# Performance work log

Measured on AMD Instinct MI355X. Metric: run time of the kernel, lower is better.

## Reference

```python
import jax, jax.numpy as jnp
import numpy as np

D = 1024        # d_hidden
DE = 512        # d_expert (routed)
E = 8           # n_routed_experts
TOP_K = 2
DS = DE * 2     # shared expert width = d_expert * n_shared_experts


def setup_inputs() -> dict:
    key = jax.random.key(0)
    ks = jax.random.split(key, 8)
    s = 1.0 / np.sqrt(D)
    return {
        "x": jax.random.normal(ks[0], (2, 1024, D), dtype=jnp.float32),
        "W_g": jax.random.normal(ks[1], (D, E), dtype=jnp.float32) * s,
        "Wg_e": jax.random.normal(ks[2], (E, D, DE), dtype=jnp.float32) * s,
        "Wu_e": jax.random.normal(ks[3], (E, D, DE), dtype=jnp.float32) * s,
        "Wd_e": jax.random.normal(ks[4], (E, DE, D), dtype=jnp.float32) * (1.0 / np.sqrt(DE)),
        "Wg_s": jax.random.normal(ks[5], (D, DS), dtype=jnp.float32) * s,
        "Wu_s": jax.random.normal(ks[6], (D, DS), dtype=jnp.float32) * s,
        "Wd_s": jax.random.normal(ks[7], (DS, D), dtype=jnp.float32) * (1.0 / np.sqrt(DS)),
    }


def _moe(x, W_g, Wg_e, Wu_e, Wd_e, Wg_s, Wu_s, Wd_s):
    B, T, Dm = x.shape
    N = B * T
    xf = x.reshape(N, Dm)

    # shared expert (SwiGLU)
    shared = (jax.nn.silu(xf @ Wg_s) * (xf @ Wu_s)) @ Wd_s  # [N, D]

    # gating: softmax then top-k (set membership identical to torch sorted=False)
    probs = jax.nn.softmax(xf @ W_g, axis=-1)               # [N, E]
    topk_vals, topk_ids = jax.lax.top_k(probs, TOP_K)       # [N, K]

    # combine weights c[n, e] = sum of topk_vals where routed to expert e
    # (equivalent to the original gather -> weighted scatter_add combine)
    c = jnp.zeros((N, E), dtype=x.dtype)
    c = c.at[jnp.arange(N)[:, None], topk_ids].add(topk_vals)

    # dense per-expert SwiGLU, weighted-combined (same math as gather/scatter loop)
    gate = jax.nn.silu(jnp.einsum('nd,edh->neh', xf, Wg_e))
    up = jnp.einsum('nd,edh->neh', xf, Wu_e)
    routed = jnp.einsum('neh,ne,ehd->nd', gate * up, c, Wd_e)  # [N, D]

    return (shared + routed).reshape(B, T, Dm)


def reference(x, W_g, Wg_e, Wu_e, Wd_e, Wg_s, Wu_s, Wd_s):
    return _moe(x, W_g, Wg_e, Wu_e, Wd_e, Wg_s, Wu_s, Wd_s)
```

## Files before the change

kernel.cpp:

```cpp
#include <hip/hip_runtime.h>
#include <hip/hip_bf16.h>

#define NTOK 2048
#define DIM  1024
#define DEXP 512
#define NEXP 8
#define DSH  1024
#define KH   5120
#define MAXROWS 5120

typedef __hip_bfloat16 bf16;
typedef __attribute__((ext_vector_type(8))) short bf16x8;
typedef __attribute__((ext_vector_type(4))) float floatx4;

__device__ __forceinline__ void gl_lds16(const bf16* g, bf16* l) {
    __builtin_amdgcn_global_load_lds(
        (const __attribute__((address_space(1))) void*)g,
        (__attribute__((address_space(3))) void*)l, 16, 0, 0);
}

__device__ __forceinline__ float b2f(short s) {
    union { float f; unsigned u; } v;
    v.u = ((unsigned)(unsigned short)s) << 16;
    return v.f;
}

struct B4 { bf16 a, b, c, d; };

__global__ __launch_bounds__(256) void gate_logits(const float* __restrict__ x,
                                                   const float* __restrict__ Wg,
                                                   bf16* __restrict__ Xb,
                                                   int2* __restrict__ te,
                                                   float2* __restrict__ tp) {
    int t = blockIdx.x * 4 + (threadIdx.x >> 6);
    int lane = threadIdx.x & 63;
    const float* xr = x + (long)t * DIM;
    bf16* xo = Xb + (long)t * DIM;
    float acc[NEXP] = {0.f, 0.f, 0.f, 0.f, 0.f, 0.f, 0.f, 0.f};
#pragma unroll
    for (int i = 0; i < 4; i++) {
        int d = lane * 4 + i * 256;
        float4 xv = *(const float4*)(xr + d);
        B4 o{__float2bfloat16(xv.x), __float2bfloat16(xv.y),
             __float2bfloat16(xv.z), __float2bfloat16(xv.w)};
        *(B4*)(xo + d) = o;
#pragma unroll
        for (int j = 0; j < 4; j++) {
            float xs = (j == 0) ? xv.x : (j == 1) ? xv.y : (j == 2) ? xv.z : xv.w;
            float4 w0 = *(const float4*)(Wg + (d + j) * NEXP);
            float4 w1 = *(const float4*)(Wg + (d + j) * NEXP + 4);
            acc[0] += xs * w0.x; acc[1] += xs * w0.y; acc[2] += xs * w0.z; acc[3] += xs * w0.w;
            acc[4] += xs * w1.x; acc[5] += xs * w1.y; acc[6] += xs * w1.z; acc[7] += xs * w1.w;
        }
    }
#pragma unroll
    for (int e = 0; e < NEXP; e++)
#pragma unroll
        for (int off = 32; off; off >>= 1)
            acc[e] += __shfl_xor(acc[e], off);
    if (lane == 0) {
        float m = acc[0];
#pragma unroll
        for (int e = 1; e < NEXP; e++) m = fmaxf(m, acc[e]);
        float p[NEXP], s = 0.f;
#pragma unroll
        for (int e = 0; e < NEXP; e++) { p[e] = expf(acc[e] - m); s += p[e]; }
        float inv = 1.f / s;
#pragma unroll
        for (int e = 0; e < NEXP; e++) p[e] *= inv;
        int i1 = 0;
#pragma unroll
        for (int e = 1; e < NEXP; e++) if (p[e] > p[i1]) i1 = e;
        int i2 = (i1 == 0) ? 1 : 0;
#pragma unroll
        for (int e = 0; e < NEXP; e++) if (e != i1 && p[e] > p[i2]) i2 = e;
        te[t] = make_int2(i1, i2);
        tp[t] = make_float2(p[i1], p[i2]);
    }
}

__global__ __launch_bounds__(512) void assign_kernel(const int2* __restrict__ te,
                                                     const float2* __restrict__ tp,
                                                     int* __restrict__ counts,
                                                     int* __restrict__ offs,
                                                     int* __restrict__ tok_list,
                                                     float* __restrict__ cw,
                                                     int* __restrict__ s1a,
                                                     int* __restrict__ s2a) {
    __shared__ int cnt[NEXP];
    const int e = threadIdx.x >> 6;
    const int lane = threadIdx.x & 63;
    int base = 0;
    for (int t0 = 0; t0 < NTOK; t0 += 64) {
        int t = t0 + lane;
        int2 ee = te[t];
        bool m1 = (ee.x == e), m2 = (ee.y == e);
        bool mt = m1 || m2;
        unsigned long long mask = __ballot(mt);
        int pre = __popcll(mask & ((1ull << lane) - 1ull));
        if (mt) {
            int slot = base + pre;
            tok_list[e * NTOK + slot] = t;
            float2 pp = tp[t];
            cw[e * NTOK + slot] = m1 ? pp.x : pp.y;
            if (m1) s1a[t] = slot; else s2a[t] = slot;
        }
        base += __popcll(mask);
    }
    if (lane == 0) cnt[e] = base;
    __syncthreads();
    if (threadIdx.x == 0) {
        int o = 0;
#pragma unroll
        for (int i = 0; i < NEXP; i++) {
            counts[i] = cnt[i];
            offs[i] = o;
            o += (cnt[i] + 127) & ~127;
        }
    }
}

__global__ __launch_bounds__(256) void pack_weights(
        const float* __restrict__ Wg_s, const float* __restrict__ Wu_s,
        const float* __restrict__ Wg_e, const float* __restrict__ Wu_e,
        const float* __restrict__ Wd_s, const float* __restrict__ Wd_e,
        bf16* __restrict__ Bg, bf16* __restrict__ Bu, bf16* __restrict__ Bd) {
    __shared__ float t[32][36];
    int b = blockIdx.x;
    const float* src; bf16* dst; int C; long dstStride, dstBase; int tilesX;
    if (b < 1024)       { src = Wg_s; dst = Bg; C = 1024; dstStride = 1024; dstBase = 0; tilesX = 32; }
    else if (b < 2048)  { b -= 1024; src = Wu_s; dst = Bu; C = 1024; dstStride = 1024; dstBase = 0; tilesX = 32; }
    else if (b < 6144)  { b -= 2048; int z = b >> 9; b &= 511;
                          src = Wg_e + (long)z * DIM * DEXP; dst = Bg; C = 512;
                          dstStride = 1024; dstBase = (long)(DSH + z * DEXP) * 1024; tilesX = 16; }
    else if (b < 10240) { b -= 6144; int z = b >> 9; b &= 511;
                          src = Wu_e + (long)z * DIM * DEXP; dst = Bu; C = 512;
                          dstStride = 1024; dstBase = (long)(DSH + z * DEXP) * 1024; tilesX = 16; }
    else if (b < 11264) { b -= 10240; src = Wd_s; dst = Bd; C = 1024; dstStride = KH; dstBase = 0; tilesX = 32; }
    else                { b -= 11264; int z = b >> 9; b &= 511;
                          src = Wd_e + (long)z * DEXP * DIM; dst = Bd; C = 1024;
                          dstStride = KH; dstBase = DSH + (long)z * DEXP; tilesX = 32; }
    int tileX = b & (tilesX - 1), tileY = b / tilesX;
    int c0 = tileX * 32, r0 = tileY * 32;

    {
        int row = threadIdx.x >> 3, ch = threadIdx.x & 7;
        float4 v = *(const float4*)(src + (long)(r0 + row) * C + c0 + ch * 4);
        *(float4*)(&t[row][ch * 4]) = v;
    }
    __syncthreads();
    {
        int dc = threadIdx.x & 31, ch = threadIdx.x >> 5;
        int j = ch * 4;
        B4 o{__float2bfloat16(t[j][dc]), __float2bfloat16(t[j + 1][dc]),
             __float2bfloat16(t[j + 2][dc]), __float2bfloat16(t[j + 3][dc])};
        *(B4*)(dst + dstBase + (long)(c0 + dc) * dstStride + r0 + j) = o;
    }
}

__global__ __launch_bounds__(256) void gu_all(const bf16* __restrict__ X,
                                              const bf16* __restrict__ Bg,
                                              const bf16* __restrict__ Bu,
                                              const int* __restrict__ counts,
                                              const int* __restrict__ offs,
                                              const int* __restrict__ tok_list,
                                              const float* __restrict__ cw,
                                              bf16* __restrict__ Hs,
                                              bf16* __restrict__ He) {
    __shared__ __align__(16) bf16 sA[128 * 32];
    __shared__ __align__(16) bf16 sBg[64 * 32];
    __shared__ __align__(16) bf16 sBu[64 * 32];

    const int b = blockIdx.x;
    const bool routed = b < 1024;
    int e = 0, m, c;
    if (routed) {
        e = b >> 7; m = (b >> 3) & 15; c = b & 7;
        if (m * 128 >= counts[e]) return;
    } else {
        int bs = b - 1024; m = bs >> 4; c = bs & 15;
    }
    const int so = routed ? offs[e] : 0;
    const int colB0 = routed ? (DSH + e * DEXP + c * 64) : c * 64;

    const int tid = threadIdx.x;
    const int wave = tid >> 6, lane = tid & 63;
    const int wr = wave >> 1, wc = wave & 1;
    const int q = lane >> 4, l15 = lane & 15;
    const int koff = (q ^ ((l15 >> 1) & 3)) * 8;

    const int r0 = tid >> 2, c4 = tid & 3;
    const int r1 = r0 + 64;
    const int c4s = c4 ^ ((r0 >> 1) & 3);
    long aRow0, aRow1;
    if (routed) {
        const int* tl = tok_list + e * NTOK + m * 128;
        aRow0 = (long)tl[r0] * DIM;
        aRow1 = (long)tl[r1] * DIM;
    } else {
        aRow0 = (long)(m * 128 + r0) * DIM;
        aRow1 = (long)(m * 128 + r1) * DIM;
    }
    const long bRow = (long)(colB0 + r0) * DIM;

    floatx4 accG[4][2], accU[4][2];
    const floatx4 z4 = {0.f, 0.f, 0.f, 0.f};
#pragma unroll
    for (int i = 0; i < 4; i++)
#pragma unroll
        for (int j = 0; j < 2; j++) { accG[i][j] = z4; accU[i][j] = z4; }

    for (int k0 = 0; k0 < DIM; k0 += 32) {
        gl_lds16(X + aRow0 + k0 + c4s * 8, sA + (wave * 64) * 8);
        gl_lds16(X + aRow1 + k0 + c4s * 8, sA + (256 + wave * 64) * 8);
        gl_lds16(Bg + bRow + k0 + c4s * 8, sBg + (wave * 64) * 8);
        gl_lds16(Bu + bRow + k0 + c4s * 8, sBu + (wave * 64) * 8);
        __syncthreads();

        bf16x8 af[4], bg[2], bu[2];
#pragma unroll
        for (int rt = 0; rt < 4; rt++)
            af[rt] = *(const bf16x8*)(sA + (wr * 64 + rt * 16 + l15) * 32 + koff);
#pragma unroll
        for (int ct = 0; ct < 2; ct++) {
            int cb = (wc * 32 + ct * 16 + l15) * 32 + koff;
            bg[ct] = *(const bf16x8*)(sBg + cb);
            bu[ct] = *(const bf16x8*)(sBu + cb);
        }
#pragma unroll
        for (int rt = 0; rt < 4; rt++)
#pragma unroll
            for (int ct = 0; ct < 2; ct++) {
                accG[rt][ct] = __builtin_amdgcn_mfma_f32_16x16x32_bf16(af[rt], bg[ct], accG[rt][ct], 0, 0, 0);
                accU[rt][ct] = __builtin_amdgcn_mfma_f32_16x16x32_bf16(af[rt], bu[ct], accU[rt][ct], 0, 0, 0);
            }
        __syncthreads();
    }

    float wv[4][4];
#pragma unroll
    for (int rt = 0; rt < 4; rt++)
#pragma unroll
        for (int r = 0; r < 4; r++) {
            int srow = wr * 64 + rt * 16 + q * 4 + r;
            wv[rt][r] = routed ? cw[e * NTOK + m * 128 + srow] : 1.0f;
        }
#pragma unroll
    for (int rt = 0; rt < 4; rt++)
#pragma unroll
        for (int ct = 0; ct < 2; ct++)
#pragma unroll
            for (int r = 0; r < 4; r++) {
                int srow = wr * 64 + rt * 16 + q * 4 + r;
                int colLoc = c * 64 + wc * 32 + ct * 16 + l15;
                float g = accG[rt][ct][r];
                float u = accU[rt][ct][r];
                float h = (g / (1.f + __expf(-g))) * u * wv[rt][r];
                if (routed)
                    He[(long)(so + m * 128 + srow) * DEXP + colLoc] = __float2bfloat16(h);
                else
                    Hs[(long)(m * 128 + srow) * DSH + colLoc] = __float2bfloat16(h);
            }
}

__global__ __launch_bounds__(256) void down_all(const bf16* __restrict__ Hs,
                                                const bf16* __restrict__ He,
                                                const bf16* __restrict__ Bd,
                                                const int* __restrict__ counts,
                                                const int* __restrict__ offs,
                                                bf16* __restrict__ Ys,
                                                bf16* __restrict__ Ye) {
    __shared__ __align__(16) bf16 sA[128 * 32];
    __shared__ __align__(16) bf16 sB[64 * 32];

    const int b = blockIdx.x;
    const bool routed = b < 2048;
    int e = 0, m, cc;
    if (routed) {
        e = b >> 8; m = (b >> 4) & 15; cc = b & 15;
        if (m * 128 >= counts[e]) return;
    } else {
        int bs = b - 2048; m = bs >> 4; cc = bs & 15;
    }
    const int so = routed ? offs[e] : 0;
    const bf16* A = routed ? He + (long)so * DEXP : Hs;
    bf16* Y = routed ? Ye + (long)so * DIM : Ys;
    const int astr = routed ? DEXP : DSH;
    const int ksteps = routed ? (DEXP / 32) : (DSH / 32);
    const int kg0 = routed ? (DSH + e * DEXP) : 0;

    const int tid = threadIdx.x;
    const int wave = tid >> 6, lane = tid & 63;
    const int wr = wave >> 1, wc = wave & 1;
    const int q = lane >> 4, l15 = lane & 15;
    const int koff = (q ^ ((l15 >> 1) & 3)) * 8;

    const int r0 = tid >> 2, c4 = tid & 3;
    const int r1 = r0 + 64;
    const int c4s = c4 ^ ((r0 >> 1) & 3);
    const long aRow0 = (long)(m * 128 + r0) * astr;
    const long aRow1 = (long)(m * 128 + r1) * astr;
    const long bRow = (long)(cc * 64 + r0) * KH + kg0;

    floatx4 acc[4][2];
    const floatx4 z4 = {0.f, 0.f, 0.f, 0.f};
#pragma unroll
    for (int i = 0; i < 4; i++)
#pragma unroll
        for (int j = 0; j < 2; j++) acc[i][j] = z4;

    for (int ks = 0; ks < ksteps; ks++) {
        const int k0 = ks * 32;
        gl_lds16(A + aRow0 + k0 + c4s * 8, sA + (wave * 64) * 8);
        gl_lds16(A + aRow1 + k0 + c4s * 8, sA + (256 + wave * 64) * 8);
        gl_lds16(Bd + bRow + k0 + c4s * 8, sB + (wave * 64) * 8);
        __syncthreads();

        bf16x8 af[4], bb[2];
#pragma unroll
        for (int rt = 0; rt < 4; rt++)
            af[rt] = *(const bf16x8*)(sA + (wr * 64 + rt * 16 + l15) * 32 + koff);
#pragma unroll
        for (int ct = 0; ct < 2; ct++)
            bb[ct] = *(const bf16x8*)(sB + (wc * 32 + ct * 16 + l15) * 32 + koff);
#pragma unroll
        for (int rt = 0; rt < 4; rt++)
#pragma unroll
            for (int ct = 0; ct < 2; ct++)
                acc[rt][ct] = __builtin_amdgcn_mfma_f32_16x16x32_bf16(af[rt], bb[ct], acc[rt][ct], 0, 0, 0);
        __syncthreads();
    }

#pragma unroll
    for (int rt = 0; rt < 4; rt++)
#pragma unroll
        for (int ct = 0; ct < 2; ct++)
#pragma unroll
            for (int r = 0; r < 4; r++) {
                int srow = wr * 64 + rt * 16 + q * 4 + r;
                int mc = cc * 64 + wc * 32 + ct * 16 + l15;
                Y[(long)(m * 128 + srow) * DIM + mc] = __float2bfloat16(acc[rt][ct][r]);
            }
}

__global__ __launch_bounds__(256) void combine_kernel(const bf16* __restrict__ Ys,
                                                      const bf16* __restrict__ Ye,
                                                      const int2* __restrict__ te,
                                                      const int* __restrict__ s1a,
                                                      const int* __restrict__ s2a,
                                                      const int* __restrict__ offs,
                                                      float* __restrict__ out) {
    int idx = blockIdx.x * 256 + threadIdx.x;
    int t = idx >> 7;
    int d = (idx & 127) * 8;
    int2 ee = te[t];
    long r1 = (long)(offs[ee.x] + s1a[t]);
    long r2 = (long)(offs[ee.y] + s2a[t]);
    bf16x8 a = *(const bf16x8*)(Ys + (long)t * DIM + d);
    bf16x8 p = *(const bf16x8*)(Ye + r1 * DIM + d);
    bf16x8 r = *(const bf16x8*)(Ye + r2 * DIM + d);
    float* o = out + (long)t * DIM + d;
#pragma unroll
    for (int i = 0; i < 8; i++)
        o[i] = b2f(a[i]) + b2f(p[i]) + b2f(r[i]);
}

extern "C" void kernel_launch(void* const* d_in, const int* in_sizes, int n_in,
                              void* d_out, int out_size, void* d_ws, size_t ws_size,
                              hipStream_t stream) {
    const float* x    = (const float*)d_in[0];
    const float* W_g  = (const float*)d_in[1];
    const float* Wg_e = (const float*)d_in[2];
    const float* Wu_e = (const float*)d_in[3];
    const float* Wd_e = (const float*)d_in[4];
    const float* Wg_s = (const float*)d_in[5];
    const float* Wu_s = (const float*)d_in[6];
    const float* Wd_s = (const float*)d_in[7];
    float* out = (float*)d_out;

    bf16* Xb = (bf16*)d_ws;
    bf16* Bg = Xb + (size_t)NTOK * DIM;
    bf16* Bu = Bg + (size_t)KH * DIM;
    bf16* Bd = Bu + (size_t)KH * DIM;
    bf16* Hs = Bd + (size_t)DIM * KH;
    bf16* He = Hs + (size_t)NTOK * DSH;
    bf16* Ys = He + (size_t)MAXROWS * DEXP;
    bf16* Ye = Ys + (size_t)NTOK * DIM;
    int*  counts   = (int*)(Ye + (size_t)MAXROWS * DIM);
    int*  offs     = counts + NEXP;
    int*  tok_list = offs + NEXP;
    float* cw      = (float*)(tok_list + NEXP * NTOK);
    int*  s1a      = (int*)(cw + NEXP * NTOK);
    int*  s2a      = s1a + NTOK;
    int2* te       = (int2*)(s2a + NTOK);
    float2* tp     = (float2*)(te + NTOK);

    hipMemsetAsync(tok_list, 0,
                   sizeof(int) * NEXP * NTOK + sizeof(float) * NEXP * NTOK, stream);
    gate_logits<<<NTOK / 4, 256, 0, stream>>>(x, W_g, Xb, te, tp);
    assign_kernel<<<1, 512, 0, stream>>>(te, tp, counts, offs, tok_list, cw, s1a, s2a);
    pack_weights<<<15360, 256, 0, stream>>>(Wg_s, Wu_s, Wg_e, Wu_e, Wd_s, Wd_e, Bg, Bu, Bd);
    gu_all<<<1280, 256, 0, stream>>>(Xb, Bg, Bu, counts, offs, tok_list, cw, Hs, He);
    down_all<<<2304, 256, 0, stream>>>(Hs, He, Bd, counts, offs, Ys, Ye);
    combine_kernel<<<NTOK * DIM / 8 / 256, 256, 0, stream>>>(Ys, Ye, te, s1a, s2a, offs, out);
}
```

Before: 208.5 us.

## Double GEMM K-tile to 64, merge gating with weight packing, drop memset

Fuses the gating/softmax/top-k kernel and the weight transpose-pack kernel into a single launch. The memset of the token list is dropped; assign_kernel now zeroes only the padding slots of each expert segment. Both grouped GEMMs move from a K-tile of 32 to 64 with a new 8-way XOR LDS swizzle. This halves the barrier count per K step and issues more async loads per sync, at the cost of twice the LDS per block.

```diff
diff --git a/kernel.cpp b/kernel.cpp
--- a/kernel.cpp
+++ b/kernel.cpp
@@ -27,55 +27,90 @@
 
 struct B4 { bf16 a, b, c, d; };
 
-__global__ __launch_bounds__(256) void gate_logits(const float* __restrict__ x,
-                                                   const float* __restrict__ Wg,
-                                                   bf16* __restrict__ Xb,
-                                                   int2* __restrict__ te,
-                                                   float2* __restrict__ tp) {
-    int t = blockIdx.x * 4 + (threadIdx.x >> 6);
-    int lane = threadIdx.x & 63;
-    const float* xr = x + (long)t * DIM;
-    bf16* xo = Xb + (long)t * DIM;
-    float acc[NEXP] = {0.f, 0.f, 0.f, 0.f, 0.f, 0.f, 0.f, 0.f};
-#pragma unroll
-    for (int i = 0; i < 4; i++) {
-        int d = lane * 4 + i * 256;
-        float4 xv = *(const float4*)(xr + d);
-        B4 o{__float2bfloat16(xv.x), __float2bfloat16(xv.y),
-             __float2bfloat16(xv.z), __float2bfloat16(xv.w)};
-        *(B4*)(xo + d) = o;
-#pragma unroll
-        for (int j = 0; j < 4; j++) {
-            float xs = (j == 0) ? xv.x : (j == 1) ? xv.y : (j == 2) ? xv.z : xv.w;
-            float4 w0 = *(const float4*)(Wg + (d + j) * NEXP);
-            float4 w1 = *(const float4*)(Wg + (d + j) * NEXP + 4);
-            acc[0] += xs * w0.x; acc[1] += xs * w0.y; acc[2] += xs * w0.z; acc[3] += xs * w0.w;
-            acc[4] += xs * w1.x; acc[5] += xs * w1.y; acc[6] += xs * w1.z; acc[7] += xs * w1.w;
-        }
-    }
-#pragma unroll
-    for (int e = 0; e < NEXP; e++)
-#pragma unroll
-        for (int off = 32; off; off >>= 1)
-            acc[e] += __shfl_xor(acc[e], off);
-    if (lane == 0) {
-        float m = acc[0];
-#pragma unroll
-        for (int e = 1; e < NEXP; e++) m = fmaxf(m, acc[e]);
-        float p[NEXP], s = 0.f;
-#pragma unroll
-        for (int e = 0; e < NEXP; e++) { p[e] = expf(acc[e] - m); s += p[e]; }
-        float inv = 1.f / s;
-#pragma unroll
-        for (int e = 0; e < NEXP; e++) p[e] *= inv;
-        int i1 = 0;
-#pragma unroll
-        for (int e = 1; e < NEXP; e++) if (p[e] > p[i1]) i1 = e;
-        int i2 = (i1 == 0) ? 1 : 0;
-#pragma unroll
-        for (int e = 0; e < NEXP; e++) if (e != i1 && p[e] > p[i2]) i2 = e;
-        te[t] = make_int2(i1, i2);
-        tp[t] = make_float2(p[i1], p[i2]);
+__global__ __launch_bounds__(256) void prep_kernel(
+        const float* __restrict__ x, const float* __restrict__ Wg,
+        const float* __restrict__ Wg_s, const float* __restrict__ Wu_s,
+        const float* __restrict__ Wg_e, const float* __restrict__ Wu_e,
+        const float* __restrict__ Wd_s, const float* __restrict__ Wd_e,
+        bf16* __restrict__ Xb, int2* __restrict__ te, float2* __restrict__ tp,
+        bf16* __restrict__ Bg, bf16* __restrict__ Bu, bf16* __restrict__ Bd) {
+    __shared__ float t[32][36];
+    if (blockIdx.x < 512) {
+        int tok = blockIdx.x * 4 + (threadIdx.x >> 6);
+        int lane = threadIdx.x & 63;
+        const float* xr = x + (long)tok * DIM;
+        bf16* xo = Xb + (long)tok * DIM;
+        float acc[NEXP] = {0.f, 0.f, 0.f, 0.f, 0.f, 0.f, 0.f, 0.f};
+#pragma unroll
+        for (int i = 0; i < 4; i++) {
+            int d = lane * 4 + i * 256;
+            float4 xv = *(const float4*)(xr + d);
+            B4 o{__float2bfloat16(xv.x), __float2bfloat16(xv.y),
+                 __float2bfloat16(xv.z), __float2bfloat16(xv.w)};
+            *(B4*)(xo + d) = o;
+#pragma unroll
+            for (int j = 0; j < 4; j++) {
+                float xs = (j == 0) ? xv.x : (j == 1) ? xv.y : (j == 2) ? xv.z : xv.w;
+                float4 w0 = *(const float4*)(Wg + (d + j) * NEXP);
+                float4 w1 = *(const float4*)(Wg + (d + j) * NEXP + 4);
+                acc[0] += xs * w0.x; acc[1] += xs * w0.y; acc[2] += xs * w0.z; acc[3] += xs * w0.w;
+                acc[4] += xs * w1.x; acc[5] += xs * w1.y; acc[6] += xs * w1.z; acc[7] += xs * w1.w;
+            }
+        }
+#pragma unroll
+        for (int e = 0; e < NEXP; e++)
+#pragma unroll
+            for (int off = 32; off; off >>= 1)
+                acc[e] += __shfl_xor(acc[e], off);
+        if (lane == 0) {
+            float m = acc[0];
+#pragma unroll
+            for (int e = 1; e < NEXP; e++) m = fmaxf(m, acc[e]);
+            float p[NEXP], s = 0.f;
+#pragma unroll
+            for (int e = 0; e < NEXP; e++) { p[e] = expf(acc[e] - m); s += p[e]; }
+            float inv = 1.f / s;
+#pragma unroll
+            for (int e = 0; e < NEXP; e++) p[e] *= inv;
+            int i1 = 0;
+#pragma unroll
+            for (int e = 1; e < NEXP; e++) if (p[e] > p[i1]) i1 = e;
+            int i2 = (i1 == 0) ? 1 : 0;
+#pragma unroll
+            for (int e = 0; e < NEXP; e++) if (e != i1 && p[e] > p[i2]) i2 = e;
+            te[tok] = make_int2(i1, i2);
+            tp[tok] = make_float2(p[i1], p[i2]);
+        }
+        return;
+    }
+    int b = blockIdx.x - 512;
+    const float* src; bf16* dst; int C; long dstStride, dstBase; int tilesX;
+    if (b < 1024)       { src = Wg_s; dst = Bg; C = 1024; dstStride = 1024; dstBase = 0; tilesX = 32; }
+    else if (b < 2048)  { b -= 1024; src = Wu_s; dst = Bu; C = 1024; dstStride = 1024; dstBase = 0; tilesX = 32; }
+    else if (b < 6144)  { b -= 2048; int z = b >> 9; b &= 511;
+                          src = Wg_e + (long)z * DIM * DEXP; dst = Bg; C = 512;
+                          dstStride = 1024; dstBase = (long)(DSH + z * DEXP) * 1024; tilesX = 16; }
+    else if (b < 10240) { b -= 6144; int z = b >> 9; b &= 511;
+                          src = Wu_e + (long)z * DIM * DEXP; dst = Bu; C = 512;
+                          dstStride = 1024; dstBase = (long)(DSH + z * DEXP) * 1024; tilesX = 16; }
+    else if (b < 11264) { b -= 10240; src = Wd_s; dst = Bd; C = 1024; dstStride = KH; dstBase = 0; tilesX = 32; }
+    else                { b -= 11264; int z = b >> 9; b &= 511;
+                          src = Wd_e + (long)z * DEXP * DIM; dst = Bd; C = 1024;
+                          dstStride = KH; dstBase = DSH + (long)z * DEXP; tilesX = 32; }
+    int tileX = b & (tilesX - 1), tileY = b / tilesX;
+    int c0 = tileX * 32, r0 = tileY * 32;
+    {
+        int row = threadIdx.x >> 3, ch = threadIdx.x & 7;
+        float4 v = *(const float4*)(src + (long)(r0 + row) * C + c0 + ch * 4);
+        *(float4*)(&t[row][ch * 4]) = v;
+    }
+    __syncthreads();
+    {
+        int dc = threadIdx.x & 31, ch = threadIdx.x >> 5;
+        int j = ch * 4;
+        B4 o{__float2bfloat16(t[j][dc]), __float2bfloat16(t[j + 1][dc]),
+             __float2bfloat16(t[j + 2][dc]), __float2bfloat16(t[j + 3][dc])};
+        *(B4*)(dst + dstBase + (long)(c0 + dc) * dstStride + r0 + j) = o;
     }
 }
 
@@ -107,6 +142,11 @@
         }
         base += __popcll(mask);
     }
+    int rc = (base + 127) & ~127;
+    for (int s = base + lane; s < rc; s += 64) {
+        tok_list[e * NTOK + s] = 0;
+        cw[e * NTOK + s] = 0.f;
+    }
     if (lane == 0) cnt[e] = base;
     __syncthreads();
     if (threadIdx.x == 0) {
@@ -117,44 +157,6 @@
             offs[i] = o;
             o += (cnt[i] + 127) & ~127;
         }
-    }
-}
-
-__global__ __launch_bounds__(256) void pack_weights(
-        const float* __restrict__ Wg_s, const float* __restrict__ Wu_s,
-        const float* __restrict__ Wg_e, const float* __restrict__ Wu_e,
-        const float* __restrict__ Wd_s, const float* __restrict__ Wd_e,
-        bf16* __restrict__ Bg, bf16* __restrict__ Bu, bf16* __restrict__ Bd) {
-    __shared__ float t[32][36];
-    int b = blockIdx.x;
-    const float* src; bf16* dst; int C; long dstStride, dstBase; int tilesX;
-    if (b < 1024)       { src = Wg_s; dst = Bg; C = 1024; dstStride = 1024; dstBase = 0; tilesX = 32; }
-    else if (b < 2048)  { b -= 1024; src = Wu_s; dst = Bu; C = 1024; dstStride = 1024; dstBase = 0; tilesX = 32; }
-    else if (b < 6144)  { b -= 2048; int z = b >> 9; b &= 511;
-                          src = Wg_e + (long)z * DIM * DEXP; dst = Bg; C = 512;
-                          dstStride = 1024; dstBase = (long)(DSH + z * DEXP) * 1024; tilesX = 16; }
-    else if (b < 10240) { b -= 6144; int z = b >> 9; b &= 511;
-                          src = Wu_e + (long)z * DIM * DEXP; dst = Bu; C = 512;
-                          dstStride = 1024; dstBase = (long)(DSH + z * DEXP) * 1024; tilesX = 16; }
-    else if (b < 11264) { b -= 10240; src = Wd_s; dst = Bd; C = 1024; dstStride = KH; dstBase = 0; tilesX = 32; }
-    else                { b -= 11264; int z = b >> 9; b &= 511;
-                          src = Wd_e + (long)z * DEXP * DIM; dst = Bd; C = 1024;
-                          dstStride = KH; dstBase = DSH + (long)z * DEXP; tilesX = 32; }
-    int tileX = b & (tilesX - 1), tileY = b / tilesX;
-    int c0 = tileX * 32, r0 = tileY * 32;
-
-    {
-        int row = threadIdx.x >> 3, ch = threadIdx.x & 7;
-        float4 v = *(const float4*)(src + (long)(r0 + row) * C + c0 + ch * 4);
-        *(float4*)(&t[row][ch * 4]) = v;
-    }
-    __syncthreads();
-    {
-        int dc = threadIdx.x & 31, ch = threadIdx.x >> 5;
-        int j = ch * 4;
-        B4 o{__float2bfloat16(t[j][dc]), __float2bfloat16(t[j + 1][dc]),
-             __float2bfloat16(t[j + 2][dc]), __float2bfloat16(t[j + 3][dc])};
-        *(B4*)(dst + dstBase + (long)(c0 + dc) * dstStride + r0 + j) = o;
     }
 }
 
@@ -167,9 +169,9 @@
                                               const float* __restrict__ cw,
                                               bf16* __restrict__ Hs,
                                               bf16* __restrict__ He) {
-    __shared__ __align__(16) bf16 sA[128 * 32];
-    __shared__ __align__(16) bf16 sBg[64 * 32];
-    __shared__ __align__(16) bf16 sBu[64 * 32];
+    __shared__ __align__(16) bf16 sA[128 * 64];
+    __shared__ __align__(16) bf16 sBg[64 * 64];
+    __shared__ __align__(16) bf16 sBu[64 * 64];
 
     const int b = blockIdx.x;
     const bool routed = b < 1024;
@@ -187,21 +189,28 @@
     const int wave = tid >> 6, lane = tid & 63;
     const int wr = wave >> 1, wc = wave & 1;
     const int q = lane >> 4, l15 = lane & 15;
-    const int koff = (q ^ ((l15 >> 1) & 3)) * 8;
-
-    const int r0 = tid >> 2, c4 = tid & 3;
-    const int r1 = r0 + 64;
-    const int c4s = c4 ^ ((r0 >> 1) & 3);
-    long aRow0, aRow1;
-    if (routed) {
-        const int* tl = tok_list + e * NTOK + m * 128;
-        aRow0 = (long)tl[r0] * DIM;
-        aRow1 = (long)tl[r1] * DIM;
-    } else {
-        aRow0 = (long)(m * 128 + r0) * DIM;
-        aRow1 = (long)(m * 128 + r1) * DIM;
-    }
-    const long bRow = (long)(colB0 + r0) * DIM;
+    const int swz = l15 & 7;
+
+    const bf16* aP[4];
+    const int* tl = tok_list + e * NTOK + m * 128;
+#pragma unroll
+    for (int j = 0; j < 4; j++) {
+        int slot = j * 256 + wave * 64 + lane;
+        int rP = slot >> 3;
+        int cP = (slot & 7) ^ (rP & 7);
+        long rowBase = routed ? (long)tl[rP] * DIM : (long)(m * 128 + rP) * DIM;
+        aP[j] = X + rowBase + cP * 8;
+    }
+    const bf16 *bgP[2], *buP[2];
+#pragma unroll
+    for (int j = 0; j < 2; j++) {
+        int slot = j * 256 + wave * 64 + lane;
+        int rP = slot >> 3;
+        int cP = (slot & 7) ^ (rP & 7);
+        long bi = (long)(colB0 + rP) * DIM + cP * 8;
+        bgP[j] = Bg + bi;
+        buP[j] = Bu + bi;
+    }
 
     floatx4 accG[4][2], accU[4][2];
     const floatx4 z4 = {0.f, 0.f, 0.f, 0.f};
@@ -210,30 +219,38 @@
 #pragma unroll
         for (int j = 0; j < 2; j++) { accG[i][j] = z4; accU[i][j] = z4; }
 
-    for (int k0 = 0; k0 < DIM; k0 += 32) {
-        gl_lds16(X + aRow0 + k0 + c4s * 8, sA + (wave * 64) * 8);
-        gl_lds16(X + aRow1 + k0 + c4s * 8, sA + (256 + wave * 64) * 8);
-        gl_lds16(Bg + bRow + k0 + c4s * 8, sBg + (wave * 64) * 8);
-        gl_lds16(Bu + bRow + k0 + c4s * 8, sBu + (wave * 64) * 8);
+    for (int k0 = 0; k0 < DIM; k0 += 64) {
+#pragma unroll
+        for (int j = 0; j < 4; j++)
+            gl_lds16(aP[j] + k0, sA + (j * 256 + wave * 64) * 8);
+#pragma unroll
+        for (int j = 0; j < 2; j++) {
+            gl_lds16(bgP[j] + k0, sBg + (j * 256 + wave * 64) * 8);
+            gl_lds16(buP[j] + k0, sBu + (j * 256 + wave * 64) * 8);
+        }
         __syncthreads();
 
-        bf16x8 af[4], bg[2], bu[2];
-#pragma unroll
-        for (int rt = 0; rt < 4; rt++)
-            af[rt] = *(const bf16x8*)(sA + (wr * 64 + rt * 16 + l15) * 32 + koff);
-#pragma unroll
-        for (int ct = 0; ct < 2; ct++) {
-            int cb = (wc * 32 + ct * 16 + l15) * 32 + koff;
-            bg[ct] = *(const bf16x8*)(sBg + cb);
-            bu[ct] = *(const bf16x8*)(sBu + cb);
-        }
-#pragma unroll
-        for (int rt = 0; rt < 4; rt++)
+#pragma unroll
+        for (int s = 0; s < 2; s++) {
+            const int p8 = ((s * 4 + q) ^ swz) * 8;
+            bf16x8 af[4], bg[2], bu[2];
+#pragma unroll
+            for (int rt = 0; rt < 4; rt++)
+                af[rt] = *(const bf16x8*)(sA + (wr * 64 + rt * 16 + l15) * 64 + p8);
 #pragma unroll
             for (int ct = 0; ct < 2; ct++) {
-                accG[rt][ct] = __builtin_amdgcn_mfma_f32_16x16x32_bf16(af[rt], bg[ct], accG[rt][ct], 0, 0, 0);
-                accU[rt][ct] = __builtin_amdgcn_mfma_f32_16x16x32_bf16(af[rt], bu[ct], accU[rt][ct], 0, 0, 0);
+                int rb = (wc * 32 + ct * 16 + l15) * 64 + p8;
+                bg[ct] = *(const bf16x8*)(sBg + rb);
+                bu[ct] = *(const bf16x8*)(sBu + rb);
             }
+#pragma unroll
+            for (int rt = 0; rt < 4; rt++)
+#pragma unroll
+                for (int ct = 0; ct < 2; ct++) {
+                    accG[rt][ct] = __builtin_amdgcn_mfma_f32_16x16x32_bf16(af[rt], bg[ct], accG[rt][ct], 0, 0, 0);
+                    accU[rt][ct] = __builtin_amdgcn_mfma_f32_16x16x32_bf16(af[rt], bu[ct], accU[rt][ct], 0, 0, 0);
+                }
+        }
         __syncthreads();
     }
 
@@ -270,8 +287,8 @@
                                                 const int* __restrict__ offs,
                                                 bf16* __restrict__ Ys,
                                                 bf16* __restrict__ Ye) {
-    __shared__ __align__(16) bf16 sA[128 * 32];
-    __shared__ __align__(16) bf16 sB[64 * 32];
+    __shared__ __align__(16) bf16 sA[128 * 64];
+    __shared__ __align__(16) bf16 sB[64 * 64];
 
     const int b = blockIdx.x;
     const bool routed = b < 2048;
@@ -286,21 +303,31 @@
     const bf16* A = routed ? He + (long)so * DEXP : Hs;
     bf16* Y = routed ? Ye + (long)so * DIM : Ys;
     const int astr = routed ? DEXP : DSH;
-    const int ksteps = routed ? (DEXP / 32) : (DSH / 32);
+    const int ksteps = routed ? (DEXP / 64) : (DSH / 64);
     const int kg0 = routed ? (DSH + e * DEXP) : 0;
 
     const int tid = threadIdx.x;
     const int wave = tid >> 6, lane = tid & 63;
     const int wr = wave >> 1, wc = wave & 1;
     const int q = lane >> 4, l15 = lane & 15;
-    const int koff = (q ^ ((l15 >> 1) & 3)) * 8;
-
-    const int r0 = tid >> 2, c4 = tid & 3;
-    const int r1 = r0 + 64;
-    const int c4s = c4 ^ ((r0 >> 1) & 3);
-    const long aRow0 = (long)(m * 128 + r0) * astr;
-    const long aRow1 = (long)(m * 128 + r1) * astr;
-    const long bRow = (long)(cc * 64 + r0) * KH + kg0;
+    const int swz = l15 & 7;
+
+    const bf16* aP[4];
+#pragma unroll
+    for (int j = 0; j < 4; j++) {
+        int slot = j * 256 + wave * 64 + lane;
+        int rP = slot >> 3;
+        int cP = (slot & 7) ^ (rP & 7);
+        aP[j] = A + (long)(m * 128 + rP) * astr + cP * 8;
+    }
+    const bf16* bP[2];
+#pragma unroll
+    for (int j = 0; j < 2; j++) {
+        int slot = j * 256 + wave * 64 + lane;
+        int rP = slot >> 3;
+        int cP = (slot & 7) ^ (rP & 7);
+        bP[j] = Bd + (long)(cc * 64 + rP) * KH + kg0 + cP * 8;
+    }
 
     floatx4 acc[4][2];
     const floatx4 z4 = {0.f, 0.f, 0.f, 0.f};
@@ -310,24 +337,31 @@
         for (int j = 0; j < 2; j++) acc[i][j] = z4;
 
     for (int ks = 0; ks < ksteps; ks++) {
-        const int k0 = ks * 32;
-        gl_lds16(A + aRow0 + k0 + c4s * 8, sA + (wave * 64) * 8);
-        gl_lds16(A + aRow1 + k0 + c4s * 8, sA + (256 + wave * 64) * 8);
-        gl_lds16(Bd + bRow + k0 + c4s * 8, sB + (wave * 64) * 8);
+        const int k0 = ks * 64;
+#pragma unroll
+        for (int j = 0; j < 4; j++)
+            gl_lds16(aP[j] + k0, sA + (j * 256 + wave * 64) * 8);
+#pragma unroll
+        for (int j = 0; j < 2; j++)
+            gl_lds16(bP[j] + k0, sB + (j * 256 + wave * 64) * 8);
         __syncthreads();
 
-        bf16x8 af[4], bb[2];
-#pragma unroll
-        for (int rt = 0; rt < 4; rt++)
-            af[rt] = *(const bf16x8*)(sA + (wr * 64 + rt * 16 + l15) * 32 + koff);
-#pragma unroll
-        for (int ct = 0; ct < 2; ct++)
-            bb[ct] = *(const bf16x8*)(sB + (wc * 32 + ct * 16 + l15) * 32 + koff);
-#pragma unroll
-        for (int rt = 0; rt < 4; rt++)
+#pragma unroll
+        for (int s = 0; s < 2; s++) {
+            const int p8 = ((s * 4 + q) ^ swz) * 8;
+            bf16x8 af[4], bb[2];
+#pragma unroll
+            for (int rt = 0; rt < 4; rt++)
+                af[rt] = *(const bf16x8*)(sA + (wr * 64 + rt * 16 + l15) * 64 + p8);
 #pragma unroll
             for (int ct = 0; ct < 2; ct++)
-                acc[rt][ct] = __builtin_amdgcn_mfma_f32_16x16x32_bf16(af[rt], bb[ct], acc[rt][ct], 0, 0, 0);
+                bb[ct] = *(const bf16x8*)(sB + (wc * 32 + ct * 16 + l15) * 64 + p8);
+#pragma unroll
+            for (int rt = 0; rt < 4; rt++)
+#pragma unroll
+                for (int ct = 0; ct < 2; ct++)
+                    acc[rt][ct] = __builtin_amdgcn_mfma_f32_16x16x32_bf16(af[rt], bb[ct], acc[rt][ct], 0, 0, 0);
+        }
         __syncthreads();
     }
 
@@ -395,11 +429,9 @@
     int2* te       = (int2*)(s2a + NTOK);
     float2* tp     = (float2*)(te + NTOK);
 
-    hipMemsetAsync(tok_list, 0,
-                   sizeof(int) * NEXP * NTOK + sizeof(float) * NEXP * NTOK, stream);
-    gate_logits<<<NTOK / 4, 256, 0, stream>>>(x, W_g, Xb, te, tp);
+    prep_kernel<<<512 + 15360, 256, 0, stream>>>(x, W_g, Wg_s, Wu_s, Wg_e, Wu_e,
+                                                 Wd_s, Wd_e, Xb, te, tp, Bg, Bu, Bd);
     assign_kernel<<<1, 512, 0, stream>>>(te, tp, counts, offs, tok_list, cw, s1a, s2a);
-    pack_weights<<<15360, 256, 0, stream>>>(Wg_s, Wu_s, Wg_e, Wu_e, Wd_s, Wd_e, Bg, Bu, Bd);
     gu_all<<<1280, 256, 0, stream>>>(Xb, Bg, Bu, counts, offs, tok_list, cw, Hs, He);
     down_all<<<2304, 256, 0, stream>>>(Hs, He, Bd, counts, offs, Ys, Ye);
     combine_kernel<<<NTOK * DIM / 8 / 256, 256, 0, stream>>>(Ys, Ye, te, s1a, s2a, offs, out);
```

Measured after the change: 212.6 us. Within noise of the previous version (+2.0%).

## Fuse MoE pipeline into one persistent cooperative kernel with grid syncs

Applied to the files above, without the earlier changes.

Merges the gating, weight packing, routing assignment, gate/up GEMM, down GEMM and combine stages into a single persistent cooperative kernel whose blocks loop over work items, with grid-wide syncs between phases. The memset is dropped; assignment now zero-fills only the padding slots. Gate and pack share one phase. This removes multiple kernel launches and the memset, at the cost of grid-sync overhead, a capped grid of at most 1024 blocks, and shared-memory reuse across phases. A multi-kernel fallback runs if the cooperative launch fails.

```diff
diff --git a/kernel.cpp b/kernel.cpp
--- a/kernel.cpp
+++ b/kernel.cpp
@@ -1,5 +1,8 @@
 #include <hip/hip_runtime.h>
+#include <hip/hip_cooperative_groups.h>
 #include <hip/hip_bf16.h>
+
+namespace cg = cooperative_groups;
 
 #define NTOK 2048
 #define DIM  1024
@@ -27,15 +30,15 @@
 
 struct B4 { bf16 a, b, c, d; };
 
-__global__ __launch_bounds__(256) void gate_logits(const float* __restrict__ x,
-                                                   const float* __restrict__ Wg,
-                                                   bf16* __restrict__ Xb,
-                                                   int2* __restrict__ te,
-                                                   float2* __restrict__ tp) {
-    int t = blockIdx.x * 4 + (threadIdx.x >> 6);
-    int lane = threadIdx.x & 63;
-    const float* xr = x + (long)t * DIM;
-    bf16* xo = Xb + (long)t * DIM;
+
+__device__ __forceinline__ void ph_gate(int gb, const float* __restrict__ x,
+                                        const float* __restrict__ Wg,
+                                        bf16* __restrict__ Xb,
+                                        int2* __restrict__ te, float2* __restrict__ tp) {
+    const int wave = threadIdx.x >> 6, lane = threadIdx.x & 63;
+    int tok = gb * 4 + wave;
+    const float* xr = x + (long)tok * DIM;
+    bf16* xo = Xb + (long)tok * DIM;
     float acc[NEXP] = {0.f, 0.f, 0.f, 0.f, 0.f, 0.f, 0.f, 0.f};
 #pragma unroll
     for (int i = 0; i < 4; i++) {
@@ -74,22 +77,50 @@
         int i2 = (i1 == 0) ? 1 : 0;
 #pragma unroll
         for (int e = 0; e < NEXP; e++) if (e != i1 && p[e] > p[i2]) i2 = e;
-        te[t] = make_int2(i1, i2);
-        tp[t] = make_float2(p[i1], p[i2]);
-    }
-}
-
-__global__ __launch_bounds__(512) void assign_kernel(const int2* __restrict__ te,
-                                                     const float2* __restrict__ tp,
-                                                     int* __restrict__ counts,
-                                                     int* __restrict__ offs,
-                                                     int* __restrict__ tok_list,
-                                                     float* __restrict__ cw,
-                                                     int* __restrict__ s1a,
-                                                     int* __restrict__ s2a) {
-    __shared__ int cnt[NEXP];
-    const int e = threadIdx.x >> 6;
-    const int lane = threadIdx.x & 63;
+        te[tok] = make_int2(i1, i2);
+        tp[tok] = make_float2(p[i1], p[i2]);
+    }
+}
+
+__device__ __forceinline__ void ph_pack(int b, float* tf,
+        const float* __restrict__ Wg_s, const float* __restrict__ Wu_s,
+        const float* __restrict__ Wg_e, const float* __restrict__ Wu_e,
+        const float* __restrict__ Wd_s, const float* __restrict__ Wd_e,
+        bf16* __restrict__ Bg, bf16* __restrict__ Bu, bf16* __restrict__ Bd) {
+    const float* src; bf16* dst; int C; long dstStride, dstBase; int tilesX;
+    if (b < 1024)       { src = Wg_s; dst = Bg; C = 1024; dstStride = 1024; dstBase = 0; tilesX = 32; }
+    else if (b < 2048)  { b -= 1024; src = Wu_s; dst = Bu; C = 1024; dstStride = 1024; dstBase = 0; tilesX = 32; }
+    else if (b < 6144)  { b -= 2048; int z = b >> 9; b &= 511;
+                          src = Wg_e + (long)z * DIM * DEXP; dst = Bg; C = 512;
+                          dstStride = 1024; dstBase = (long)(DSH + z * DEXP) * 1024; tilesX = 16; }
+    else if (b < 10240) { b -= 6144; int z = b >> 9; b &= 511;
+                          src = Wu_e + (long)z * DIM * DEXP; dst = Bu; C = 512;
+                          dstStride = 1024; dstBase = (long)(DSH + z * DEXP) * 1024; tilesX = 16; }
+    else if (b < 11264) { b -= 10240; src = Wd_s; dst = Bd; C = 1024; dstStride = KH; dstBase = 0; tilesX = 32; }
+    else                { b -= 11264; int z = b >> 9; b &= 511;
+                          src = Wd_e + (long)z * DEXP * DIM; dst = Bd; C = 1024;
+                          dstStride = KH; dstBase = DSH + (long)z * DEXP; tilesX = 32; }
+    int tileX = b & (tilesX - 1), tileY = b / tilesX;
+    int c0 = tileX * 32, tr0 = tileY * 32;
+    {
+        int row = threadIdx.x >> 3, ch = threadIdx.x & 7;
+        float4 v = *(const float4*)(src + (long)(tr0 + row) * C + c0 + ch * 4);
+        *(float4*)(&tf[row * 36 + ch * 4]) = v;
+    }
+    __syncthreads();
+    {
+        int dc = threadIdx.x & 31, ch = threadIdx.x >> 5;
+        int j = ch * 4;
+        B4 o{__float2bfloat16(tf[j * 36 + dc]),       __float2bfloat16(tf[(j + 1) * 36 + dc]),
+             __float2bfloat16(tf[(j + 2) * 36 + dc]), __float2bfloat16(tf[(j + 3) * 36 + dc])};
+        *(B4*)(dst + dstBase + (long)(c0 + dc) * dstStride + tr0 + j) = o;
+    }
+}
+
+__device__ __forceinline__ int ph_assign(int e, int lane,
+        const int2* __restrict__ te, const float2* __restrict__ tp,
+        int* __restrict__ tok_list, float* __restrict__ cw,
+        int* __restrict__ s1a, int* __restrict__ s2a) {
     int base = 0;
     for (int t0 = 0; t0 < NTOK; t0 += 64) {
         int t = t0 + lane;
@@ -107,71 +138,19 @@
         }
         base += __popcll(mask);
     }
-    if (lane == 0) cnt[e] = base;
-    __syncthreads();
-    if (threadIdx.x == 0) {
-        int o = 0;
-#pragma unroll
-        for (int i = 0; i < NEXP; i++) {
-            counts[i] = cnt[i];
-            offs[i] = o;
-            o += (cnt[i] + 127) & ~127;
-        }
-    }
-}
-
-__global__ __launch_bounds__(256) void pack_weights(
-        const float* __restrict__ Wg_s, const float* __restrict__ Wu_s,
-        const float* __restrict__ Wg_e, const float* __restrict__ Wu_e,
-        const float* __restrict__ Wd_s, const float* __restrict__ Wd_e,
-        bf16* __restrict__ Bg, bf16* __restrict__ Bu, bf16* __restrict__ Bd) {
-    __shared__ float t[32][36];
-    int b = blockIdx.x;
-    const float* src; bf16* dst; int C; long dstStride, dstBase; int tilesX;
-    if (b < 1024)       { src = Wg_s; dst = Bg; C = 1024; dstStride = 1024; dstBase = 0; tilesX = 32; }
-    else if (b < 2048)  { b -= 1024; src = Wu_s; dst = Bu; C = 1024; dstStride = 1024; dstBase = 0; tilesX = 32; }
-    else if (b < 6144)  { b -= 2048; int z = b >> 9; b &= 511;
-                          src = Wg_e + (long)z * DIM * DEXP; dst = Bg; C = 512;
-                          dstStride = 1024; dstBase = (long)(DSH + z * DEXP) * 1024; tilesX = 16; }
-    else if (b < 10240) { b -= 6144; int z = b >> 9; b &= 511;
-                          src = Wu_e + (long)z * DIM * DEXP; dst = Bu; C = 512;
-                          dstStride = 1024; dstBase = (long)(DSH + z * DEXP) * 1024; tilesX = 16; }
-    else if (b < 11264) { b -= 10240; src = Wd_s; dst = Bd; C = 1024; dstStride = KH; dstBase = 0; tilesX = 32; }
-    else                { b -= 11264; int z = b >> 9; b &= 511;
-                          src = Wd_e + (long)z * DEXP * DIM; dst = Bd; C = 1024;
-                          dstStride = KH; dstBase = DSH + (long)z * DEXP; tilesX = 32; }
-    int tileX = b & (tilesX - 1), tileY = b / tilesX;
-    int c0 = tileX * 32, r0 = tileY * 32;
-
-    {
-        int row = threadIdx.x >> 3, ch = threadIdx.x & 7;
-        float4 v = *(const float4*)(src + (long)(r0 + row) * C + c0 + ch * 4);
-        *(float4*)(&t[row][ch * 4]) = v;
-    }
-    __syncthreads();
-    {
-        int dc = threadIdx.x & 31, ch = threadIdx.x >> 5;
-        int j = ch * 4;
-        B4 o{__float2bfloat16(t[j][dc]), __float2bfloat16(t[j + 1][dc]),
-             __float2bfloat16(t[j + 2][dc]), __float2bfloat16(t[j + 3][dc])};
-        *(B4*)(dst + dstBase + (long)(c0 + dc) * dstStride + r0 + j) = o;
-    }
-}
-
-__global__ __launch_bounds__(256) void gu_all(const bf16* __restrict__ X,
-                                              const bf16* __restrict__ Bg,
-                                              const bf16* __restrict__ Bu,
-                                              const int* __restrict__ counts,
-                                              const int* __restrict__ offs,
-                                              const int* __restrict__ tok_list,
-                                              const float* __restrict__ cw,
-                                              bf16* __restrict__ Hs,
-                                              bf16* __restrict__ He) {
-    __shared__ __align__(16) bf16 sA[128 * 32];
-    __shared__ __align__(16) bf16 sBg[64 * 32];
-    __shared__ __align__(16) bf16 sBu[64 * 32];
-
-    const int b = blockIdx.x;
+    int rc = (base + 127) & ~127;
+    for (int s = base + lane; s < rc; s += 64) {
+        tok_list[e * NTOK + s] = 0;
+        cw[e * NTOK + s] = 0.f;
+    }
+    return base;
+}
+
+__device__ __forceinline__ void ph_gu(int b, bf16* sA, bf16* sB0, bf16* sB1,
+        const bf16* __restrict__ X, const bf16* __restrict__ Bg, const bf16* __restrict__ Bu,
+        const int* __restrict__ counts, const int* __restrict__ offs,
+        const int* __restrict__ tok_list, const float* __restrict__ cw,
+        bf16* __restrict__ Hs, bf16* __restrict__ He) {
     const bool routed = b < 1024;
     int e = 0, m, c;
     if (routed) {
@@ -182,13 +161,11 @@
     }
     const int so = routed ? offs[e] : 0;
     const int colB0 = routed ? (DSH + e * DEXP + c * 64) : c * 64;
-
     const int tid = threadIdx.x;
     const int wave = tid >> 6, lane = tid & 63;
     const int wr = wave >> 1, wc = wave & 1;
     const int q = lane >> 4, l15 = lane & 15;
     const int koff = (q ^ ((l15 >> 1) & 3)) * 8;
-
     const int r0 = tid >> 2, c4 = tid & 3;
     const int r1 = r0 + 64;
     const int c4s = c4 ^ ((r0 >> 1) & 3);
@@ -213,8 +190,8 @@
     for (int k0 = 0; k0 < DIM; k0 += 32) {
         gl_lds16(X + aRow0 + k0 + c4s * 8, sA + (wave * 64) * 8);
         gl_lds16(X + aRow1 + k0 + c4s * 8, sA + (256 + wave * 64) * 8);
-        gl_lds16(Bg + bRow + k0 + c4s * 8, sBg + (wave * 64) * 8);
-        gl_lds16(Bu + bRow + k0 + c4s * 8, sBu + (wave * 64) * 8);
+        gl_lds16(Bg + bRow + k0 + c4s * 8, sB0 + (wave * 64) * 8);
+        gl_lds16(Bu + bRow + k0 + c4s * 8, sB1 + (wave * 64) * 8);
         __syncthreads();
 
         bf16x8 af[4], bg[2], bu[2];
@@ -224,8 +201,8 @@
 #pragma unroll
         for (int ct = 0; ct < 2; ct++) {
             int cb = (wc * 32 + ct * 16 + l15) * 32 + koff;
-            bg[ct] = *(const bf16x8*)(sBg + cb);
-            bu[ct] = *(const bf16x8*)(sBu + cb);
+            bg[ct] = *(const bf16x8*)(sB0 + cb);
+            bu[ct] = *(const bf16x8*)(sB1 + cb);
         }
 #pragma unroll
         for (int rt = 0; rt < 4; rt++)
@@ -263,17 +240,11 @@
             }
 }
 
-__global__ __launch_bounds__(256) void down_all(const bf16* __restrict__ Hs,
-                                                const bf16* __restrict__ He,
-                                                const bf16* __restrict__ Bd,
-                                                const int* __restrict__ counts,
-                                                const int* __restrict__ offs,
-                                                bf16* __restrict__ Ys,
-                                                bf16* __restrict__ Ye) {
-    __shared__ __align__(16) bf16 sA[128 * 32];
-    __shared__ __align__(16) bf16 sB[64 * 32];
-
-    const int b = blockIdx.x;
+__device__ __forceinline__ void ph_down(int b, bf16* sA, bf16* sB0,
+        const bf16* __restrict__ Hs, const bf16* __restrict__ He,
+        const bf16* __restrict__ Bd,
+        const int* __restrict__ counts, const int* __restrict__ offs,
+        bf16* __restrict__ Ys, bf16* __restrict__ Ye) {
     const bool routed = b < 2048;
     int e = 0, m, cc;
     if (routed) {
@@ -288,13 +259,11 @@
     const int astr = routed ? DEXP : DSH;
     const int ksteps = routed ? (DEXP / 32) : (DSH / 32);
     const int kg0 = routed ? (DSH + e * DEXP) : 0;
-
     const int tid = threadIdx.x;
     const int wave = tid >> 6, lane = tid & 63;
     const int wr = wave >> 1, wc = wave & 1;
     const int q = lane >> 4, l15 = lane & 15;
     const int koff = (q ^ ((l15 >> 1) & 3)) * 8;
-
     const int r0 = tid >> 2, c4 = tid & 3;
     const int r1 = r0 + 64;
     const int c4s = c4 ^ ((r0 >> 1) & 3);
@@ -313,7 +282,7 @@
         const int k0 = ks * 32;
         gl_lds16(A + aRow0 + k0 + c4s * 8, sA + (wave * 64) * 8);
         gl_lds16(A + aRow1 + k0 + c4s * 8, sA + (256 + wave * 64) * 8);
-        gl_lds16(Bd + bRow + k0 + c4s * 8, sB + (wave * 64) * 8);
+        gl_lds16(Bd + bRow + k0 + c4s * 8, sB0 + (wave * 64) * 8);
         __syncthreads();
 
         bf16x8 af[4], bb[2];
@@ -322,7 +291,7 @@
             af[rt] = *(const bf16x8*)(sA + (wr * 64 + rt * 16 + l15) * 32 + koff);
 #pragma unroll
         for (int ct = 0; ct < 2; ct++)
-            bb[ct] = *(const bf16x8*)(sB + (wc * 32 + ct * 16 + l15) * 32 + koff);
+            bb[ct] = *(const bf16x8*)(sB0 + (wc * 32 + ct * 16 + l15) * 32 + koff);
 #pragma unroll
         for (int rt = 0; rt < 4; rt++)
 #pragma unroll
@@ -343,26 +312,135 @@
             }
 }
 
-__global__ __launch_bounds__(256) void combine_kernel(const bf16* __restrict__ Ys,
-                                                      const bf16* __restrict__ Ye,
-                                                      const int2* __restrict__ te,
-                                                      const int* __restrict__ s1a,
-                                                      const int* __restrict__ s2a,
-                                                      const int* __restrict__ offs,
-                                                      float* __restrict__ out) {
-    int idx = blockIdx.x * 256 + threadIdx.x;
+__device__ __forceinline__ void ph_combine(int idx,
+        const bf16* __restrict__ Ys, const bf16* __restrict__ Ye,
+        const int2* __restrict__ te, const int* __restrict__ s1a,
+        const int* __restrict__ s2a, const int* __restrict__ offs,
+        float* __restrict__ out) {
     int t = idx >> 7;
     int d = (idx & 127) * 8;
     int2 ee = te[t];
-    long r1 = (long)(offs[ee.x] + s1a[t]);
-    long r2 = (long)(offs[ee.y] + s2a[t]);
+    long rr1 = (long)(offs[ee.x] + s1a[t]);
+    long rr2 = (long)(offs[ee.y] + s2a[t]);
     bf16x8 a = *(const bf16x8*)(Ys + (long)t * DIM + d);
-    bf16x8 p = *(const bf16x8*)(Ye + r1 * DIM + d);
-    bf16x8 r = *(const bf16x8*)(Ye + r2 * DIM + d);
+    bf16x8 p = *(const bf16x8*)(Ye + rr1 * DIM + d);
+    bf16x8 r = *(const bf16x8*)(Ye + rr2 * DIM + d);
     float* o = out + (long)t * DIM + d;
 #pragma unroll
     for (int i = 0; i < 8; i++)
         o[i] = b2f(a[i]) + b2f(p[i]) + b2f(r[i]);
+}
+
+__global__ __launch_bounds__(256, 3) void moe_coop(
+        const float* __restrict__ x, const float* __restrict__ Wg,
+        const float* __restrict__ Wg_s, const float* __restrict__ Wu_s,
+        const float* __restrict__ Wg_e, const float* __restrict__ Wu_e,
+        const float* __restrict__ Wd_s, const float* __restrict__ Wd_e,
+        bf16* __restrict__ Xb, int2* __restrict__ te, float2* __restrict__ tp,
+        bf16* __restrict__ Bg, bf16* __restrict__ Bu, bf16* __restrict__ Bd,
+        int* __restrict__ counts, int* __restrict__ offs,
+        int* __restrict__ tok_list, float* __restrict__ cw,
+        int* __restrict__ s1a, int* __restrict__ s2a,
+        bf16* __restrict__ Hs, bf16* __restrict__ He,
+        bf16* __restrict__ Ys, bf16* __restrict__ Ye,
+        float* __restrict__ out) {
+    cg::grid_group grid = cg::this_grid();
+    __shared__ __align__(16) bf16 smem[8192];
+    __shared__ int scnt[NEXP];
+    bf16* sA = smem;
+    bf16* sB0 = smem + 4096;
+    bf16* sB1 = smem + 6144;
+
+    for (int wb = blockIdx.x; wb < 512 + 15360; wb += gridDim.x) {
+        if (wb < 512) ph_gate(wb, x, Wg, Xb, te, tp);
+        else ph_pack(wb - 512, (float*)smem, Wg_s, Wu_s, Wg_e, Wu_e, Wd_s, Wd_e, Bg, Bu, Bd);
+        __syncthreads();
+    }
+    grid.sync();
+
+    if (blockIdx.x == 0) {
+        const int wave = threadIdx.x >> 6, lane = threadIdx.x & 63;
+#pragma unroll
+        for (int eo = 0; eo < 2; eo++) {
+            int e = wave * 2 + eo;
+            int cnt = ph_assign(e, lane, te, tp, tok_list, cw, s1a, s2a);
+            if (lane == 0) scnt[e] = cnt;
+        }
+        __syncthreads();
+        if (threadIdx.x == 0) {
+            int o = 0;
+#pragma unroll
+            for (int i = 0; i < NEXP; i++) {
+                counts[i] = scnt[i];
+                offs[i] = o;
+                o += (scnt[i] + 127) & ~127;
+            }
+        }
+    }
+    grid.sync();
+
+    for (int b = blockIdx.x; b < 1280; b += gridDim.x)
+        ph_gu(b, sA, sB0, sB1, Xb, Bg, Bu, counts, offs, tok_list, cw, Hs, He);
+    grid.sync();
+
+    for (int b = blockIdx.x; b < 2304; b += gridDim.x)
+        ph_down(b, sA, sB0, Hs, He, Bd, counts, offs, Ys, Ye);
+    grid.sync();
+
+    for (int idx = blockIdx.x * 256 + threadIdx.x; idx < NTOK * DIM / 8;
+         idx += gridDim.x * 256)
+        ph_combine(idx, Ys, Ye, te, s1a, s2a, offs, out);
+}
+
+__global__ __launch_bounds__(256) void prep_kernel(
+        const float* x, const float* Wg,
+        const float* Wg_s, const float* Wu_s, const float* Wg_e, const float* Wu_e,
+        const float* Wd_s, const float* Wd_e,
+        bf16* Xb, int2* te, float2* tp, bf16* Bg, bf16* Bu, bf16* Bd) {
+    __shared__ __align__(16) float tf[32 * 36];
+    if (blockIdx.x < 512) ph_gate(blockIdx.x, x, Wg, Xb, te, tp);
+    else ph_pack(blockIdx.x - 512, tf, Wg_s, Wu_s, Wg_e, Wu_e, Wd_s, Wd_e, Bg, Bu, Bd);
+}
+
+__global__ __launch_bounds__(512) void assign_kernel(
+        const int2* te, const float2* tp, int* counts, int* offs,
+        int* tok_list, float* cw, int* s1a, int* s2a) {
+    __shared__ int scnt[NEXP];
+    const int e = threadIdx.x >> 6, lane = threadIdx.x & 63;
+    int cnt = ph_assign(e, lane, te, tp, tok_list, cw, s1a, s2a);
+    if (lane == 0) scnt[e] = cnt;
+    __syncthreads();
+    if (threadIdx.x == 0) {
+        int o = 0;
+#pragma unroll
+        for (int i = 0; i < NEXP; i++) {
+            counts[i] = scnt[i];
+            offs[i] = o;
+            o += (scnt[i] + 127) & ~127;
+        }
+    }
+}
+
+__global__ __launch_bounds__(256) void gu_kernel(
+        const bf16* X, const bf16* Bg, const bf16* Bu,
+        const int* counts, const int* offs, const int* tok_list, const float* cw,
+        bf16* Hs, bf16* He) {
+    __shared__ __align__(16) bf16 smem[8192];
+    ph_gu(blockIdx.x, smem, smem + 4096, smem + 6144, X, Bg, Bu,
+          counts, offs, tok_list, cw, Hs, He);
+}
+
+__global__ __launch_bounds__(256) void down_kernel(
+        const bf16* Hs, const bf16* He, const bf16* Bd,
+        const int* counts, const int* offs, bf16* Ys, bf16* Ye) {
+    __shared__ __align__(16) bf16 smem[6144];
+    ph_down(blockIdx.x, smem, smem + 4096, Hs, He, Bd, counts, offs, Ys, Ye);
+}
+
+__global__ __launch_bounds__(256) void combine_kernel(
+        const bf16* Ys, const bf16* Ye, const int2* te,
+        const int* s1a, const int* s2a, const int* offs, float* out) {
+    ph_combine(blockIdx.x * 256 + threadIdx.x, Ys, Ye, te, s1a, s2a, offs, out);
 }
 
 extern "C" void kernel_launch(void* const* d_in, const int* in_sizes, int n_in,
@@ -395,12 +473,30 @@
     int2* te       = (int2*)(s2a + NTOK);
     float2* tp     = (float2*)(te + NTOK);
 
-    hipMemsetAsync(tok_list, 0,
-                   sizeof(int) * NEXP * NTOK + sizeof(float) * NEXP * NTOK, stream);
-    gate_logits<<<NTOK / 4, 256, 0, stream>>>(x, W_g, Xb, te, tp);
-    assign_kernel<<<1, 512, 0, stream>>>(te, tp, counts, offs, tok_list, cw, s1a, s2a);
-    pack_weights<<<15360, 256, 0, stream>>>(Wg_s, Wu_s, Wg_e, Wu_e, Wd_s, Wd_e, Bg, Bu, Bd);
-    gu_all<<<1280, 256, 0, stream>>>(Xb, Bg, Bu, counts, offs, tok_list, cw, Hs, He);
-    down_all<<<2304, 256, 0, stream>>>(Hs, He, Bd, counts, offs, Ys, Ye);
-    combine_kernel<<<NTOK * DIM / 8 / 256, 256, 0, stream>>>(Ys, Ye, te, s1a, s2a, offs, out);
-}
+    bool coop_ok = false;
+    int maxB = 0;
+    hipError_t qerr = hipOccupancyMaxActiveBlocksPerMultiprocessor(&maxB, moe_coop, 256, 0);
+    if (qerr == hipSuccess && maxB > 0) {
+        int grid = maxB * 256;
+        if (grid > 1024) grid = 1024;
+        void* args[] = {
+            (void*)&x, (void*)&W_g, (void*)&Wg_s, (void*)&Wu_s, (void*)&Wg_e, (void*)&Wu_e,
+            (void*)&Wd_s, (void*)&Wd_e, (void*)&Xb, (void*)&te, (void*)&tp,
+            (void*)&Bg, (void*)&Bu, (void*)&Bd, (void*)&counts, (void*)&offs,
+            (void*)&tok_list, (void*)&cw, (void*)&s1a, (void*)&s2a,
+            (void*)&Hs, (void*)&He, (void*)&Ys, (void*)&Ye, (void*)&out
+        };
+        hipError_t lerr = hipLaunchCooperativeKernel((void*)moe_coop, dim3(grid),
+                                                     dim3(256), args, 0, stream);
+        coop_ok = (lerr == hipSuccess);
+    }
+
+    if (!coop_ok) {
+        prep_kernel<<<512 + 15360, 256, 0, stream>>>(x, W_g, Wg_s, Wu_s, Wg_e, Wu_e,
+                                                     Wd_s, Wd_e, Xb, te, tp, Bg, Bu, Bd);
+        assign_kernel<<<1, 512, 0, stream>>>(te, tp, counts, offs, tok_list, cw, s1a, s2a);
+        gu_kernel<<<1280, 256, 0, stream>>>(Xb, Bg, Bu, counts, offs, tok_list, cw, Hs, He);
+        down_kernel<<<2304, 256, 0, stream>>>(Hs, He, Bd, counts, offs, Ys, Ye);
+        combine_kernel<<<NTOK * DIM / 8 / 256, 256, 0, stream>>>(Ys, Ye, te, s1a, s2a, offs, out);
+    }
+}
```

Result: slower. 496.5 us (+138.1%).
